# Kernel optimization log

Measured on AMD Instinct MI355X. Metric: run time of the kernel, lower is better.

## Reference

```python
import jax, jax.numpy as jnp
import numpy as np

R = 64  # all tensor-ring ranks equal

def setup_inputs() -> dict:
    key = jax.random.key(0)
    k1, k2, k3 = jax.random.split(key, 3)
    B, T, N, M, C = 512, 64, 512, 64, 100
    # xavier-uniform-ish scale for weights (gain=init_value=1.0)
    s_sh = float(np.sqrt(6.0 / (R * N + R)))
    s_la = float(np.sqrt(6.0 / (C * R * M + R)))
    return {
        "tensor": jax.random.normal(k1, (B, T, N), dtype=jnp.float32),
        "W_shared": jax.random.uniform(k2, (R, N, R), dtype=jnp.float32, minval=-s_sh, maxval=s_sh),
        "W_last": jax.random.uniform(k3, (C, R, M, R), dtype=jnp.float32, minval=-s_la, maxval=s_la),
    }

def reference(tensor, W_shared, W_last):
    B = tensor.shape[0]
    xt = jnp.transpose(tensor, (1, 0, 2))  # [T, B, N]
    state0 = jnp.ones((R, B, R), dtype=tensor.dtype)  # [r1, B, r2]
    # per-step: x = einsum('bj,rbi->rbji'); state = einsum('ijk,rbji->rbk')
    # == einsum('bj,rbi,ijk->rbk'); factored to avoid the [r,b,n,r] intermediate
    def step(state, x_t):
        bik = jnp.einsum('bj,ijk->bik', x_t, W_shared)   # [B, r2, r3]
        new = jnp.einsum('rbi,bik->rbk', state, bik)     # [r1, B, r3]
        return new, None
    state, _ = jax.lax.scan(step, state0, xt)
    # last kernel with pad_input = ones(B, m):
    # einsum('cijk,rbji->cbrk') with x[r,b,j,i]=state[r,b,i] == sum over j of W_last
    W_sum = jnp.sum(W_last, axis=2)                      # [C, r2, r_last]
    state = jnp.einsum('cik,rbi->cbrk', W_sum, state)    # [C, B, r1, r_last]
    # trace over the last two (square) rank dims
    out = jnp.einsum('cbrr->cb', state)                  # [C, B]
    return out
```

## Files before the change

### kernel.cpp

```cpp
#include <hip/hip_runtime.h>
#include <hip/hip_fp16.h>


typedef _Float16 f16;
typedef __attribute__((ext_vector_type(8))) _Float16 f16x8;
typedef __attribute__((ext_vector_type(2))) _Float16 f16x2;
typedef __attribute__((ext_vector_type(4))) float f32x4;

#define GLDS16(g, l)                                                      \
    __builtin_amdgcn_global_load_lds(                                     \
        (const __attribute__((address_space(1))) void*)(g),               \
        (__attribute__((address_space(3))) void*)(l), 16, 0, 0)

#define BARRIER() asm volatile("s_barrier" ::: "memory")
#define VMCNT(n) asm volatile("s_waitcnt vmcnt(" #n ")" ::: "memory")

__global__ __launch_bounds__(256) void k_usum(const float* __restrict__ Wl,
                                              float* __restrict__ u) {
    int ci = blockIdx.x;
    const float4* p = (const float4*)(Wl + (size_t)ci * 4096);
    int tid = threadIdx.x;
    float s = 0.f;
#pragma unroll
    for (int q = 0; q < 4; ++q) {
        float4 v = p[tid + 256 * q];
        s += v.x + v.y + v.z + v.w;
    }
    __shared__ float red[256];
    red[tid] = s;
    __syncthreads();
    if (tid < 128) red[tid] += red[tid + 128];
    __syncthreads();
    if (tid < 64) {
        float x = red[tid] + red[tid + 64];
#pragma unroll
        for (int off = 32; off > 0; off >>= 1) x += __shfl_down(x, off, 64);
        if (tid == 0) u[ci] = x;
    }
}

__global__ __launch_bounds__(256) void k_cvtA(const float* __restrict__ in,
                                              f16* __restrict__ out) {
    int idx = blockIdx.x * 256 + threadIdx.x;
    const float4* p = (const float4*)in + (size_t)idx * 2;
    float4 v0 = p[0], v1 = p[1];
    f16x8 h;
    h[0] = (f16)v0.x; h[1] = (f16)v0.y; h[2] = (f16)v0.z; h[3] = (f16)v0.w;
    h[4] = (f16)v1.x; h[5] = (f16)v1.y; h[6] = (f16)v1.z; h[7] = (f16)v1.w;
    *(f16x8*)(out + (size_t)idx * 8) = h;
}

__global__ __launch_bounds__(256) void k_cvtW(const float* __restrict__ W,
                                              f16* __restrict__ Bt) {
    int o = blockIdx.x * 256 + threadIdx.x;
    int col = o >> 8;
    int j = (o & 255) << 1;
    int i = col >> 6, k = col & 63;
    const float* src = W + ((size_t)i * 512 + j) * 64 + k;
    f16x2 pk;
    pk[0] = (f16)src[0];
    pk[1] = (f16)src[64];
    *(f16x2*)(Bt + (size_t)col * 512 + j) = pk;
}


#define STAGE_A(qq, ha, ktv) do {                                             \
    _Pragma("unroll") for (int u_ = 0; u_ < 2; ++u_) {                        \
        int idx_ = (wid * 2 + u_) * 64 + lane;                                \
        int r_ = idx_ >> 3;                                                   \
        int ls_ = (idx_ & 7) ^ (r_ & 7);                                      \
        const f16* g_ = A + (size_t)(m0 + (ha) * 128 + r_) * 512              \
                          + (ktv) * 64 + ls_ * 8;                             \
        char* l_ = smem + (qq) * 65536 + (ha) * 16384 + (wid * 2 + u_) * 1024;\
        GLDS16(g_, l_);                                                       \
    } } while (0)

#define STAGE_B(qq, hb, ktv) do {                                             \
    _Pragma("unroll") for (int u_ = 0; u_ < 2; ++u_) {                        \
        int idx_ = (wid * 2 + u_) * 64 + lane;                                \
        int r_ = idx_ >> 3;                                                   \
        int ls_ = (idx_ & 7) ^ (r_ & 7);                                      \
        const f16* g_ = Bt + (size_t)(n0 + (hb) * 128 + r_) * 512             \
                           + (ktv) * 64 + ls_ * 8;                            \
        char* l_ = smem + (qq) * 65536 + 32768 + (hb) * 16384                 \
                        + (wid * 2 + u_) * 1024;                              \
        GLDS16(g_, l_);                                                       \
    } } while (0)

#define RD_A(ha, ktv) do {                                                    \
    _Pragma("unroll") for (int mf_ = 0; mf_ < 4; ++mf_)                       \
    _Pragma("unroll") for (int kq_ = 0; kq_ < 2; ++kq_) {                     \
        int ra_ = wr * 64 + mf_ * 16 + (lane & 15);                           \
        int off_ = ((ra_ << 7) + kq_ * 64 + ((lane >> 4) << 4))               \
                   ^ ((ra_ & 7) << 4);                                        \
        a[mf_][kq_] = *(const f16x8*)(smem + ((ktv) & 1) * 65536              \
                                      + (ha) * 16384 + off_);                 \
    } } while (0)

#define RD_B(hb, ktv, breg) do {                                              \
    _Pragma("unroll") for (int nf_ = 0; nf_ < 2; ++nf_)                       \
    _Pragma("unroll") for (int kq_ = 0; kq_ < 2; ++kq_) {                     \
        int rb_ = wc * 32 + nf_ * 16 + (lane & 15);                           \
        int off_ = ((rb_ << 7) + kq_ * 64 + ((lane >> 4) << 4))               \
                   ^ ((rb_ & 7) << 4);                                        \
        breg[nf_][kq_] = *(const f16x8*)(smem + ((ktv) & 1) * 65536           \
                                         + 32768 + (hb) * 16384 + off_);      \
    } } while (0)

#define MFMA_Q(qa_, qb_, breg) do {                                           \
    __builtin_amdgcn_s_setprio(1);                                            \
    _Pragma("unroll") for (int mf_ = 0; mf_ < 4; ++mf_)                       \
    _Pragma("unroll") for (int nf_ = 0; nf_ < 2; ++nf_)                       \
    _Pragma("unroll") for (int kq_ = 0; kq_ < 2; ++kq_)                       \
        acc[qa_][qb_][mf_][nf_] = __builtin_amdgcn_mfma_f32_16x16x32_f16(     \
            a[mf_][kq_], breg[nf_][kq_], acc[qa_][qb_][mf_][nf_], 0, 0, 0);   \
    __builtin_amdgcn_s_setprio(0);                                            \
    } while (0)

__global__ __launch_bounds__(512) void k_gemm_256(const f16* __restrict__ A,
                                                  const f16* __restrict__ Bt,
                                                  __half* __restrict__ outp) {
    extern __shared__ char smem[];
    const int tid = threadIdx.x;
    const int lane = tid & 63;
    const int wid = tid >> 6;
    int lin = blockIdx.x;
    int swz = (lin & 7) * 256 + (lin >> 3);
    const int n0 = (swz & 15) * 256;
    const int m0 = (swz >> 4) * 256;
    const int wr = wid >> 2, wc = wid & 3;

    f32x4 acc[2][2][4][2];
#pragma unroll
    for (int x = 0; x < 2; ++x)
#pragma unroll
        for (int y = 0; y < 2; ++y)
#pragma unroll
            for (int z = 0; z < 4; ++z)
#pragma unroll
                for (int w = 0; w < 2; ++w) acc[x][y][z][w] = (f32x4)0.f;

    f16x8 a[4][2], b0[2][2], b1[2][2];

    STAGE_A(0, 0, 0);
    STAGE_B(0, 0, 0);
    STAGE_B(0, 1, 0);
    STAGE_A(0, 1, 0);
    STAGE_A(1, 0, 1);
    STAGE_B(1, 0, 1);
    STAGE_B(1, 1, 1);

    for (int kt = 0; kt < 6; ++kt) {
        VMCNT(6);
        BARRIER();
        RD_A(0, kt);
        RD_B(0, kt, b0);
        STAGE_A((kt + 1) & 1, 1, kt + 1);
        MFMA_Q(0, 0, b0);
        BARRIER();
        RD_B(1, kt, b1);
        MFMA_Q(0, 1, b1);
        BARRIER();
        RD_A(1, kt);
        STAGE_A(kt & 1, 0, kt + 2);
        STAGE_B(kt & 1, 0, kt + 2);
        MFMA_Q(1, 0, b0);
        BARRIER();
        STAGE_B(kt & 1, 1, kt + 2);
        MFMA_Q(1, 1, b1);
        BARRIER();
    }
    {
        VMCNT(6);
        BARRIER();
        RD_A(0, 6);
        RD_B(0, 6, b0);
        STAGE_A(1, 1, 7);
        MFMA_Q(0, 0, b0);
        BARRIER();
        RD_B(1, 6, b1);
        MFMA_Q(0, 1, b1);
        BARRIER();
        RD_A(1, 6);
        MFMA_Q(1, 0, b0);
        BARRIER();
        MFMA_Q(1, 1, b1);
        BARRIER();
    }
    {
        VMCNT(0);
        BARRIER();
        RD_A(0, 7);
        RD_B(0, 7, b0);
        MFMA_Q(0, 0, b0);
        BARRIER();
        RD_B(1, 7, b1);
        MFMA_Q(0, 1, b1);
        BARRIER();
        RD_A(1, 7);
        MFMA_Q(1, 0, b0);
        BARRIER();
        MFMA_Q(1, 1, b1);
        BARRIER();
    }

    __half* Cs = (__half*)smem;
#pragma unroll
    for (int qa = 0; qa < 2; ++qa)
#pragma unroll
        for (int qb = 0; qb < 2; ++qb)
#pragma unroll
            for (int mf = 0; mf < 4; ++mf)
#pragma unroll
                for (int nf = 0; nf < 2; ++nf)
#pragma unroll
                    for (int j = 0; j < 4; ++j) {
                        int row = qa * 128 + wr * 64 + mf * 16 + ((lane >> 4) << 2) + j;
                        int col = qb * 128 + wc * 32 + nf * 16 + (lane & 15);
                        Cs[row * 256 + col] = __float2half(acc[qa][qb][mf][nf][j]);
                    }
    BARRIER();
#pragma unroll
    for (int it = 0; it < 16; ++it) {
        int idx = it * 512 + tid;
        int r = idx >> 5, seg = idx & 31;
        *(float4*)(outp + (size_t)(m0 + r) * 4096 + n0 + seg * 8) =
            *(const float4*)(Cs + r * 256 + seg * 8);
    }
}

#define BM 128
#define BN 64
#define BK 32
__global__ __launch_bounds__(256) void k_gemm(const float* __restrict__ A,
                                              const float* __restrict__ W,
                                              __half* __restrict__ out,
                                              int a_off, int a_stride) {
    __shared__ float As[BK * BM];
    __shared__ float Bs[BK * BN];
    int i0 = blockIdx.x;
    int m0 = blockIdx.y * BM;
    int tid = threadIdx.x;
    int tx = tid & 15, ty = tid >> 4;
    float acc[8][4];
#pragma unroll
    for (int q = 0; q < 8; ++q)
#pragma unroll
        for (int c = 0; c < 4; ++c) acc[q][c] = 0.f;
    const float* wbase = W + (size_t)i0 * 32768;
    for (int j0 = 0; j0 < 512; j0 += BK) {
        {
            int c4 = tid & 7;
            int r = tid >> 3;
#pragma unroll
            for (int p = 0; p < 4; ++p) {
                int row = r + 32 * p;
                float4 v = *(const float4*)(A + (size_t)a_off +
                                            (size_t)(m0 + row) * a_stride + j0 + 4 * c4);
                As[(4 * c4 + 0) * BM + row] = v.x;
                As[(4 * c4 + 1) * BM + row] = v.y;
                As[(4 * c4 + 2) * BM + row] = v.z;
                As[(4 * c4 + 3) * BM + row] = v.w;
            }
            const float4* src = (const float4*)(wbase + (size_t)j0 * 64);
            float4* dst = (float4*)Bs;
            dst[tid] = src[tid];
            dst[tid + 256] = src[tid + 256];
        }
        __syncthreads();
#pragma unroll
        for (int kk = 0; kk < BK; ++kk) {
            float bv[4], av[8];
#pragma unroll
            for (int c = 0; c < 4; ++c) bv[c] = Bs[kk * BN + 4 * tx + c];
#pragma unroll
            for (int q = 0; q < 8; ++q) av[q] = As[kk * BM + 8 * ty + q];
#pragma unroll
            for (int q = 0; q < 8; ++q)
#pragma unroll
                for (int c = 0; c < 4; ++c) acc[q][c] += av[q] * bv[c];
        }
        __syncthreads();
    }
#pragma unroll
    for (int q = 0; q < 8; ++q) {
        int m = m0 + 8 * ty + q;
        __half* o = out + (size_t)m * 4096 + i0 * 64 + 4 * tx;
#pragma unroll
        for (int c = 0; c < 4; ++c) o[c] = __float2half(acc[q][c]);
    }
}

__global__ __launch_bounds__(256) void k_scan(const __half* __restrict__ bik,
                                              const float* __restrict__ u,
                                              float* __restrict__ out) {
    int b = blockIdx.x;
    int tid = threadIdx.x;
    int k = tid & 63, grp = tid >> 6;
    __shared__ float vsh[64];
    __shared__ float part[256];
    if (tid < 64) vsh[tid] = 1.0f;
    const __half* base = bik + (size_t)b * 64 * 4096 + grp * 16 * 64 + k;
    __half bufA[16], bufB[16];
#pragma unroll
    for (int q = 0; q < 16; ++q) bufA[q] = base[q * 64];
    __syncthreads();
    for (int t = 0; t < 64; t += 2) {
        {
            const __half* pn = base + (size_t)(t + 1) * 4096;
#pragma unroll
            for (int q = 0; q < 16; ++q) bufB[q] = pn[q * 64];
            float s = 0.f;
#pragma unroll
            for (int q = 0; q < 16; ++q) s += vsh[grp * 16 + q] * __half2float(bufA[q]);
            part[tid] = s;
            __syncthreads();
            if (tid < 64) vsh[k] = part[k] + part[64 + k] + part[128 + k] + part[192 + k];
            __syncthreads();
        }
        {
            int t2 = (t + 2 < 64) ? (t + 2) : 63;
            const __half* pn = base + (size_t)t2 * 4096;
#pragma unroll
            for (int q = 0; q < 16; ++q) bufA[q] = pn[q * 64];
            float s = 0.f;
#pragma unroll
            for (int q = 0; q < 16; ++q) s += vsh[grp * 16 + q] * __half2float(bufB[q]);
            part[tid] = s;
            __syncthreads();
            if (tid < 64) vsh[k] = part[k] + part[64 + k] + part[128 + k] + part[192 + k];
            __syncthreads();
        }
    }
    if (tid < 100) {
        const float* uc = u + tid * 64;
        float s = 0.f;
#pragma unroll 8
        for (int i = 0; i < 64; ++i) s += uc[i] * vsh[i];
        out[tid * 512 + b] = s;
    }
}

__global__ __launch_bounds__(256) void k_update(const __half* __restrict__ Mt,
                                                const float* __restrict__ vin,
                                                float* __restrict__ vout, int first) {
    int o = blockIdx.x * 256 + threadIdx.x;
    int b = o >> 6, k = o & 63;
    const __half* m = Mt + (size_t)b * 4096;
    float s = 0.f;
    if (first) {
#pragma unroll 8
        for (int i = 0; i < 64; ++i) s += __half2float(m[i * 64 + k]);
    } else {
        const float* v = vin + (size_t)b * 64;
#pragma unroll 8
        for (int i = 0; i < 64; ++i) s += v[i] * __half2float(m[i * 64 + k]);
    }
    vout[o] = s;
}

__global__ __launch_bounds__(256) void k_final(const float* __restrict__ u,
                                               const float* __restrict__ v,
                                               float* __restrict__ out) {
    int o = blockIdx.x * 256 + threadIdx.x;
    int c = o >> 9, b = o & 511;
    const float* uc = u + c * 64;
    const float* vb = v + (size_t)b * 64;
    float s = 0.f;
#pragma unroll 8
    for (int i = 0; i < 64; ++i) s += uc[i] * vb[i];
    out[o] = s;
}

extern "C" void kernel_launch(void* const* d_in, const int* in_sizes, int n_in,
                              void* d_out, int out_size, void* d_ws, size_t ws_size,
                              hipStream_t stream) {
    const float* tensor = (const float*)d_in[0];
    const float* Wsh = (const float*)d_in[1];
    const float* Wl = (const float*)d_in[2];
    float* out = (float*)d_out;
    char* ws = (char*)d_ws;

    const size_t bik_bytes = (size_t)32768 * 4096 * sizeof(__half);
    const size_t fast_bytes = bik_bytes + (512u << 10) + ((size_t)16777216 * 2) + ((size_t)4096 * 512 * 2);

    if (ws_size >= fast_bytes) {
        __half* bik = (__half*)ws;
        float* u = (float*)(ws + bik_bytes);
        f16* Af16 = (f16*)(ws + bik_bytes + (512u << 10));
        f16* Btw = Af16 + (size_t)16777216;

        k_cvtA<<<8192, 256, 0, stream>>>(tensor, Af16);
        k_cvtW<<<4096, 256, 0, stream>>>(Wsh, Btw);
        k_usum<<<6400, 256, 0, stream>>>(Wl, u);
        (void)hipFuncSetAttribute((const void*)k_gemm_256,
                                  hipFuncAttributeMaxDynamicSharedMemorySize, 131072);
        k_gemm_256<<<2048, 512, 131072, stream>>>(Af16, Btw, bik);
        k_scan<<<512, 256, 0, stream>>>(bik, u, out);
    } else if (ws_size >= bik_bytes + (2u << 20)) {
        __half* bik = (__half*)ws;
        float* u = (float*)(ws + bik_bytes);

        k_usum<<<6400, 256, 0, stream>>>(Wl, u);
        dim3 g(64, 256);
        k_gemm<<<g, 256, 0, stream>>>(tensor, Wsh, bik, 0, 512);
        k_scan<<<512, 256, 0, stream>>>(bik, u, out);
    } else {
        __half* bikt = (__half*)ws;
        float* u = (float*)(ws + (size_t)(4 << 20));
        float* v0 = (float*)(ws + (size_t)(4 << 20) + (64 << 10));
        float* v1 = v0 + 32768;

        k_usum<<<6400, 256, 0, stream>>>(Wl, u);
        for (int t = 0; t < 64; ++t) {
            dim3 g(64, 4);
            k_gemm<<<g, 256, 0, stream>>>(tensor, Wsh, bikt, t * 512, 32768);
            float* vin = (t & 1) ? v0 : v1;
            float* vout = (t & 1) ? v1 : v0;
            k_update<<<128, 256, 0, stream>>>(bikt, (t == 0) ? v0 : vin, vout, t == 0);
        }
        k_final<<<200, 256, 0, stream>>>(u, v1, out);
    }
}
```

Before: 282.8 us.

## Double-buffer A fragments and restructure GEMM pipeline with finer vmcnt waits

Splits the A register fragments into two sets so LDS reads for the next quadrant overlap with MFMAs on the current one. It also reorders global-to-LDS staging so each half-tile is issued one step ahead, with finer vmcnt waits instead of one wait per iteration. The block-index swizzle is changed to group tiles into 8x8 super-tiles for better L2 reuse. This adds register pressure from the second A buffer and depends on the new wait counts exactly covering the outstanding loads.

Result: slower. 421.2 us (+48.9%).

```diff
diff --git a/kernel.cpp b/kernel.cpp
--- a/kernel.cpp
+++ b/kernel.cpp
@@ -87,14 +87,14 @@
         GLDS16(g_, l_);                                                       \
     } } while (0)
 
-#define RD_A(ha, ktv) do {                                                    \
+#define RD_A(ha, ktv, areg) do {                                              \
     _Pragma("unroll") for (int mf_ = 0; mf_ < 4; ++mf_)                       \
     _Pragma("unroll") for (int kq_ = 0; kq_ < 2; ++kq_) {                     \
         int ra_ = wr * 64 + mf_ * 16 + (lane & 15);                           \
         int off_ = ((ra_ << 7) + kq_ * 64 + ((lane >> 4) << 4))               \
                    ^ ((ra_ & 7) << 4);                                        \
-        a[mf_][kq_] = *(const f16x8*)(smem + ((ktv) & 1) * 65536              \
-                                      + (ha) * 16384 + off_);                 \
+        areg[mf_][kq_] = *(const f16x8*)(smem + ((ktv) & 1) * 65536           \
+                                         + (ha) * 16384 + off_);              \
     } } while (0)
 
 #define RD_B(hb, ktv, breg) do {                                              \
@@ -107,13 +107,13 @@
                                          + 32768 + (hb) * 16384 + off_);      \
     } } while (0)
 
-#define MFMA_Q(qa_, qb_, breg) do {                                           \
+#define MFMA_Q(qa_, qb_, areg, breg) do {                                     \
     __builtin_amdgcn_s_setprio(1);                                            \
     _Pragma("unroll") for (int mf_ = 0; mf_ < 4; ++mf_)                       \
     _Pragma("unroll") for (int nf_ = 0; nf_ < 2; ++nf_)                       \
     _Pragma("unroll") for (int kq_ = 0; kq_ < 2; ++kq_)                       \
         acc[qa_][qb_][mf_][nf_] = __builtin_amdgcn_mfma_f32_16x16x32_f16(     \
-            a[mf_][kq_], breg[nf_][kq_], acc[qa_][qb_][mf_][nf_], 0, 0, 0);   \
+            areg[mf_][kq_], breg[nf_][kq_], acc[qa_][qb_][mf_][nf_], 0, 0, 0);\
     __builtin_amdgcn_s_setprio(0);                                            \
     } while (0)
 
@@ -125,22 +125,24 @@
     const int lane = tid & 63;
     const int wid = tid >> 6;
     int lin = blockIdx.x;
-    int swz = (lin & 7) * 256 + (lin >> 3);
-    const int n0 = (swz & 15) * 256;
-    const int m0 = (swz >> 4) * 256;
+    int x = lin & 7, q = lin >> 3;
+    int st = 4 * x + (q >> 6);
+    int sub = q & 63;
+    const int m0 = ((st >> 1) * 8 + (sub >> 3)) * 256;
+    const int n0 = ((st & 1) * 8 + (sub & 7)) * 256;
     const int wr = wid >> 2, wc = wid & 3;
 
     f32x4 acc[2][2][4][2];
 #pragma unroll
-    for (int x = 0; x < 2; ++x)
-#pragma unroll
-        for (int y = 0; y < 2; ++y)
-#pragma unroll
-            for (int z = 0; z < 4; ++z)
-#pragma unroll
-                for (int w = 0; w < 2; ++w) acc[x][y][z][w] = (f32x4)0.f;
-
-    f16x8 a[4][2], b0[2][2], b1[2][2];
+    for (int xx = 0; xx < 2; ++xx)
+#pragma unroll
+        for (int yy = 0; yy < 2; ++yy)
+#pragma unroll
+            for (int zz = 0; zz < 4; ++zz)
+#pragma unroll
+                for (int ww = 0; ww < 2; ++ww) acc[xx][yy][zz][ww] = (f32x4)0.f;
+
+    f16x8 a0[4][2], a1[4][2], b0[2][2], b1[2][2];
 
     STAGE_A(0, 0, 0);
     STAGE_B(0, 0, 0);
@@ -148,61 +150,64 @@
     STAGE_A(0, 1, 0);
     STAGE_A(1, 0, 1);
     STAGE_B(1, 0, 1);
+    VMCNT(8);
+    BARRIER();
+    RD_A(0, 0, a0);
+    RD_B(0, 0, b0);
+    VMCNT(4);
+    BARRIER();
+
+    RD_B(1, 0, b1);
+    MFMA_Q(0, 0, a0, b0);
+    BARRIER();
+    RD_A(1, 0, a1);
+    MFMA_Q(0, 1, a0, b1);
+    BARRIER();
     STAGE_B(1, 1, 1);
-
-    for (int kt = 0; kt < 6; ++kt) {
-        VMCNT(6);
+    STAGE_A(1, 1, 1);
+    MFMA_Q(1, 0, a1, b0);
+    VMCNT(4);
+    BARRIER();
+    RD_A(0, 1, a0);
+    RD_B(0, 1, b0);
+    MFMA_Q(1, 1, a1, b1);
+    VMCNT(2);
+    BARRIER();
+
+#pragma unroll
+    for (int kt = 1; kt < 7; ++kt) {
+        RD_B(1, kt, b1);
+        STAGE_A((kt + 1) & 1, 0, kt + 1);
+        STAGE_B((kt + 1) & 1, 0, kt + 1);
+        MFMA_Q(0, 0, a0, b0);
+        VMCNT(4);
         BARRIER();
-        RD_A(0, kt);
-        RD_B(0, kt, b0);
+        RD_A(1, kt, a1);
+        MFMA_Q(0, 1, a0, b1);
+        BARRIER();
+        STAGE_B((kt + 1) & 1, 1, kt + 1);
         STAGE_A((kt + 1) & 1, 1, kt + 1);
-        MFMA_Q(0, 0, b0);
+        MFMA_Q(1, 0, a1, b0);
+        VMCNT(4);
         BARRIER();
-        RD_B(1, kt, b1);
-        MFMA_Q(0, 1, b1);
+        RD_A(0, kt + 1, a0);
+        RD_B(0, kt + 1, b0);
+        MFMA_Q(1, 1, a1, b1);
+        VMCNT(2);
         BARRIER();
-        RD_A(1, kt);
-        STAGE_A(kt & 1, 0, kt + 2);
-        STAGE_B(kt & 1, 0, kt + 2);
-        MFMA_Q(1, 0, b0);
-        BARRIER();
-        STAGE_B(kt & 1, 1, kt + 2);
-        MFMA_Q(1, 1, b1);
-        BARRIER();
-    }
-    {
-        VMCNT(6);
-        BARRIER();
-        RD_A(0, 6);
-        RD_B(0, 6, b0);
-        STAGE_A(1, 1, 7);
-        MFMA_Q(0, 0, b0);
-        BARRIER();
-        RD_B(1, 6, b1);
-        MFMA_Q(0, 1, b1);
-        BARRIER();
-        RD_A(1, 6);
-        MFMA_Q(1, 0, b0);
-        BARRIER();
-        MFMA_Q(1, 1, b1);
-        BARRIER();
-    }
-    {
-        VMCNT(0);
-        BARRIER();
-        RD_A(0, 7);
-        RD_B(0, 7, b0);
-        MFMA_Q(0, 0, b0);
-        BARRIER();
-        RD_B(1, 7, b1);
-        MFMA_Q(0, 1, b1);
-        BARRIER();
-        RD_A(1, 7);
-        MFMA_Q(1, 0, b0);
-        BARRIER();
-        MFMA_Q(1, 1, b1);
-        BARRIER();
-    }
+    }
+
+    RD_B(1, 7, b1);
+    MFMA_Q(0, 0, a0, b0);
+    VMCNT(0);
+    BARRIER();
+    RD_A(1, 7, a1);
+    MFMA_Q(0, 1, a0, b1);
+    BARRIER();
+    MFMA_Q(1, 0, a1, b0);
+    BARRIER();
+    MFMA_Q(1, 1, a1, b1);
+    BARRIER();
 
     __half* Cs = (__half*)smem;
 #pragma unroll
```
